# Performance work log

Hardware: AMD Instinct MI355X
Metric: run time of the kernel (lower is better)

## Reference

```python
import jax, jax.numpy as jnp
import numpy as np

B, S, D, H = 2, 2048, 1024, 16
DEPTH = D // H


def setup_inputs() -> dict:
    key = jax.random.key(0)
    ks = jax.random.split(key, 12)
    sc = 1.0 / np.sqrt(D)
    n = lambda k, shp, s=sc: jax.random.normal(k, shp, dtype=jnp.float32) * s
    return {
        "q": jax.random.normal(ks[0], (B, S, D), dtype=jnp.float32),
        "k": jax.random.normal(ks[1], (B, S, D), dtype=jnp.float32),
        "v": jax.random.normal(ks[2], (B, S, D), dtype=jnp.float32),
        # key-padding mask: 1 = masked, 0 = keep (added to logits * -1e9)
        "mask": (jax.random.uniform(ks[3], (B, 1, 1, S)) < 0.1).astype(jnp.float32),
        "wq_w": n(ks[4], (D, D)), "wq_b": jnp.zeros((D,), jnp.float32),
        "wk_w": n(ks[5], (D, D)), "wk_b": jnp.zeros((D,), jnp.float32),
        "wv_w": n(ks[6], (D, D)), "wv_b": jnp.zeros((D,), jnp.float32),
        "dense_w": n(ks[7], (D, D)), "dense_b": jnp.zeros((D,), jnp.float32),
    }


def _split_heads(x, b, s):
    # [B, S, D] -> [B, H, S, depth]
    return x.reshape(b, s, H, DEPTH).transpose(0, 2, 1, 3)


def reference(q, k, v, mask, wq_w, wq_b, wk_w, wk_b, wv_w, wv_b, dense_w, dense_b):
    b, sq, _ = q.shape
    sk = k.shape[1]
    qh = _split_heads(q @ wq_w.T + wq_b, b, sq)
    kh = _split_heads(k @ wk_w.T + wk_b, b, sk)
    vh = _split_heads(v @ wv_w.T + wv_b, b, sk)
    scale = 1.0 / jnp.sqrt(jnp.float32(DEPTH))
    logits = jnp.einsum('bhqd,bhkd->bhqk', qh, kh) * scale  # [B,H,Sq,Sk]
    logits = logits + mask * (-1e9)
    attn = jax.nn.softmax(logits, axis=-1)
    ctx = jnp.einsum('bhqk,bhkd->bhqd', attn, vh)
    ctx = ctx.transpose(0, 2, 1, 3).reshape(b, sq, D)  # concat heads
    out = ctx @ dense_w.T + dense_b
    return out, attn
```

## Files before the change

### kernel.cpp

```cpp
#include <hip/hip_runtime.h>

#define BB 2
#define SS 2048
#define DD 1024
#define HH 16
#define DEPTH 64
#define MTOT (BB*SS)
#define QW 8
#define QBLK (QW*16)
#define NT (SS/64)
#define NT2 (SS/128)
#define NPROJ ((size_t)BB*HH*SS*DEPTH)
#define WSZ   ((size_t)DD*DD)

using f16 = _Float16;
typedef _Float16 f16x8 __attribute__((ext_vector_type(8)));
typedef _Float16 f16x4 __attribute__((ext_vector_type(4)));
typedef float f32x4 __attribute__((ext_vector_type(4)));

#define LOG2E 1.44269504088896f
#define SC2   (0.125f * LOG2E)

#define GLOAD16(g, l) __builtin_amdgcn_global_load_lds(                      \
    (__attribute__((address_space(1))) const void*)(g),                      \
    (__attribute__((address_space(3))) void*)(l), 16, 0, 0)

#define BARV(N) do {                                                         \
    __builtin_amdgcn_sched_barrier(0);                                       \
    asm volatile("s_waitcnt vmcnt(" #N ") lgkmcnt(0)" ::: "memory");         \
    __builtin_amdgcn_sched_barrier(0);                                       \
    __builtin_amdgcn_s_barrier();                                            \
    __builtin_amdgcn_sched_barrier(0);                                       \
} while (0)

__global__ __launch_bounds__(256) void cvt_kernel(
    const float* __restrict__ q, const float* __restrict__ k, const float* __restrict__ v,
    const float* __restrict__ w0, const float* __restrict__ w1, const float* __restrict__ w2,
    f16* __restrict__ qf, f16* __restrict__ kf, f16* __restrict__ vf,
    f16* __restrict__ wq, f16* __restrict__ wk, f16* __restrict__ wv)
{
    const int z = blockIdx.y;
    const float* s = z==0?q : z==1?k : z==2?v : z==3?w0 : z==4?w1 : w2;
    f16*        d = z==0?qf: z==1?kf: z==2?vf: z==3?wq: z==4?wk: wv;
    const size_t n = (z < 3) ? NPROJ : WSZ;
    for (size_t i = ((size_t)blockIdx.x * 256 + threadIdx.x) * 8; i < n;
         i += (size_t)gridDim.x * 256 * 8) {
        f32x4 a = *(const f32x4*)(s + i);
        f32x4 b = *(const f32x4*)(s + i + 4);
        f16x8 o = {(f16)a[0], (f16)a[1], (f16)a[2], (f16)a[3],
                   (f16)b[0], (f16)b[1], (f16)b[2], (f16)b[3]};
        *(f16x8*)(d + i) = o;
    }
}

__global__ __launch_bounds__(256) void cvt2_kernel(
    const float* __restrict__ s, f16* __restrict__ d)
{
    size_t i = ((size_t)blockIdx.x * 256 + threadIdx.x) * 8;
    if (i < WSZ) {
        f32x4 a = *(const f32x4*)(s + i);
        f32x4 b = *(const f32x4*)(s + i + 4);
        f16x8 o = {(f16)a[0], (f16)a[1], (f16)a[2], (f16)a[3],
                   (f16)b[0], (f16)b[1], (f16)b[2], (f16)b[3]};
        *(f16x8*)(d + i) = o;
    }
}

__global__ __launch_bounds__(256, 4) void proj_kernel(
    const f16* __restrict__ qf, const f16* __restrict__ kf, const f16* __restrict__ vf,
    const f16* __restrict__ wqw, const f16* __restrict__ wkw, const f16* __restrict__ wvw,
    const float* __restrict__ bq, const float* __restrict__ bk, const float* __restrict__ bv,
    f16* __restrict__ qh, f16* __restrict__ kh, f16* __restrict__ vt)
{
    const int mode = blockIdx.z;
    const f16* A    = mode==0 ? qf  : mode==1 ? kf  : vf;
    const f16* Bw   = mode==0 ? wqw : mode==1 ? wkw : wvw;
    const float* bias = mode==0 ? bq : mode==1 ? bk : bv;

    __shared__ f16 As[128*64];
    __shared__ f16 Bs[128*64];

    const int tid = threadIdx.x, wave = tid >> 6, lane = tid & 63;
    const int m0 = blockIdx.y * 128, n0 = blockIdx.x * 128;
    const int wm = (wave >> 1) * 64, wn = (wave & 1) * 64;
    const int lrow = lane & 15, g = lane >> 4;
    const int sw = lrow & 7;
    const int srow = tid >> 3;
    const int schk = (tid & 7) ^ (srow & 7);

    f32x4 acc[4][4] = {};

    for (int kk = 0; kk < DD; kk += 64) {
        #pragma unroll
        for (int i = 0; i < 4; ++i) {
            GLOAD16(A  + (size_t)(m0 + i*32 + srow) * DD + kk + schk * 8,
                    &As[i*2048 + wave*512]);
            GLOAD16(Bw + (size_t)(n0 + i*32 + srow) * DD + kk + schk * 8,
                    &Bs[i*2048 + wave*512]);
        }
        __syncthreads();
        for (int kf2 = 0; kf2 < 2; ++kf2) {
            f16x8 a[4], bf[4];
            for (int i = 0; i < 4; ++i)
                a[i]  = *(const f16x8*)&As[(wm + i*16 + lrow)*64 + ((kf2*4 + g) ^ sw)*8];
            for (int i = 0; i < 4; ++i)
                bf[i] = *(const f16x8*)&Bs[(wn + i*16 + lrow)*64 + ((kf2*4 + g) ^ sw)*8];
            for (int mi = 0; mi < 4; ++mi)
                for (int ni = 0; ni < 4; ++ni)
                    acc[mi][ni] = __builtin_amdgcn_mfma_f32_16x16x32_f16(a[mi], bf[ni], acc[mi][ni], 0, 0, 0);
        }
        __syncthreads();
    }

    const int rbase = g * 4;
    if (mode == 2) {
        for (int ni = 0; ni < 4; ++ni) {
            int n = n0 + wn + ni * 16 + lrow;
            float bval = bias[n];
            int hh = n >> 6, dep = n & 63;
            for (int mi = 0; mi < 4; ++mi) {
                int m = m0 + wm + mi * 16 + rbase;
                int bb = m >> 11, s = m & 2047;
                f16x4 pk = {(f16)(acc[mi][ni][0] + bval), (f16)(acc[mi][ni][1] + bval),
                            (f16)(acc[mi][ni][2] + bval), (f16)(acc[mi][ni][3] + bval)};
                *(f16x4*)&vt[((size_t)(bb * HH + hh) * DEPTH + dep) * SS + s] = pk;
            }
        }
    } else {
        f16* dst = (mode == 0) ? qh : kh;
        for (int ni = 0; ni < 4; ++ni) {
            int n = n0 + wn + ni * 16 + lrow;
            float bval = bias[n];
            int hh = n >> 6, dep = n & 63;
            for (int mi = 0; mi < 4; ++mi)
                for (int j = 0; j < 4; ++j) {
                    int m = m0 + wm + mi * 16 + rbase + j;
                    int bb = m >> 11, s = m & 2047;
                    dst[((size_t)(bb * HH + hh) * SS + s) * DEPTH + dep] = (f16)(acc[mi][ni][j] + bval);
                }
        }
    }
}

__global__ __launch_bounds__(512, 4) void attn_kernel(
    const f16* __restrict__ qh, const f16* __restrict__ kh, const f16* __restrict__ vt,
    const float* __restrict__ mask, float* __restrict__ attn_out, f16* __restrict__ ctx)
{
    __shared__ unsigned char mflag[SS];
    __shared__ f16 Ks[3][64*64];
    __shared__ f16 Vs[3][64*64];
    __shared__ f16 Pl[QW][16][72];

    const int tid = threadIdx.x, wave = tid >> 6, lane = tid & 63;
    const int L = blockIdx.x;
    const int xcd = L & 7, iw = L >> 3;
    const int bh = xcd * 4 + (iw >> 4);
    const int qb = iw & 15;
    const int b = bh >> 4, h = bh & 15;
    const int q0 = qb * QBLK;
    const int lrow = lane & 15, g = lane >> 4;
    const int rbase = g * 4;
    const int sw = lrow & 7;
    const int srow = tid >> 3;
    const int schk = (tid & 7) ^ (srow & 7);

    const f16* Qbase = qh + (size_t)bh * SS * DEPTH;
    const f16* Kb = kh + (size_t)bh * SS * DEPTH;
    const f16* Vb = vt + (size_t)bh * DEPTH * SS;

    for (int i = tid; i < SS; i += 512)
        mflag[i] = mask[b * SS + i] > 0.5f ? 1 : 0;

    f16x8 aq[2];
    for (int kf2 = 0; kf2 < 2; ++kf2)
        aq[kf2] = *(const f16x8*)(Qbase + (size_t)(q0 + wave*16 + lrow) * DEPTH + kf2*32 + g*8);

    float s_l[4] = {0.f, 0.f, 0.f, 0.f};
    GLOAD16(Kb + (size_t)(srow) * DEPTH + schk * 8,        &Ks[0][wave * 512]);
    GLOAD16(Kb + (size_t)(64 + srow) * DEPTH + schk * 8,   &Vs[0][wave * 512]);
    GLOAD16(Kb + (size_t)(128 + srow) * DEPTH + schk * 8,  &Ks[1][wave * 512]);
    GLOAD16(Kb + (size_t)(192 + srow) * DEPTH + schk * 8,  &Vs[1][wave * 512]);
    __syncthreads();
    for (int t = 0; t < NT2; ++t) {
        const int cur = t % 3;
        const int nxt = (t + 2) % 3;
        const int t2 = (t + 2) & (NT2 - 1);
        GLOAD16(Kb + (size_t)(t2*128 + srow) * DEPTH + schk * 8,      &Ks[nxt][wave * 512]);
        GLOAD16(Kb + (size_t)(t2*128 + 64 + srow) * DEPTH + schk * 8, &Vs[nxt][wave * 512]);
        #pragma unroll
        for (int nf = 0; nf < 8; ++nf) {
            const f16* tb = (nf < 4) ? &Ks[cur][0] : &Vs[cur][0];
            const int nfl = nf & 3;
            f32x4 a4 = {};
            for (int kf2 = 0; kf2 < 2; ++kf2) {
                f16x8 bf = *(const f16x8*)&tb[(nfl*16 + lrow)*64 + ((kf2*4 + g) ^ sw)*8];
                a4 = __builtin_amdgcn_mfma_f32_16x16x32_f16(aq[kf2], bf, a4, 0, 0, 0);
            }
            float sel = mflag[t*128 + nf*16 + lrow] ? 0.f : 1.f;
            for (int j = 0; j < 4; ++j)
                s_l[j] += sel * __builtin_amdgcn_exp2f(a4[j] * SC2);
        }
        if (t < NT2 - 1) BARV(2);
        else __syncthreads();
    }
    for (int j = 0; j < 4; ++j) {
        float s = s_l[j];
        for (int off = 1; off < 16; off <<= 1) s += __shfl_xor(s, off);
        s_l[j] = 1.0f / s;
    }

    f32x4 cacc[4] = {};
    f32x4 st[4];
    float* arow = attn_out + ((size_t)bh * SS + q0 + wave * 16) * SS;
    GLOAD16(Kb + (size_t)(srow) * DEPTH + schk * 8,        &Ks[0][wave * 512]);
    GLOAD16(Vb + (size_t)srow * SS + 0 + schk * 8,         &Vs[0][wave * 512]);
    GLOAD16(Kb + (size_t)(64 + srow) * DEPTH + schk * 8,   &Ks[1][wave * 512]);
    GLOAD16(Vb + (size_t)srow * SS + 64 + schk * 8,        &Vs[1][wave * 512]);
    __syncthreads();
    for (int kt = 0; kt < NT; ++kt) {
        const int cur = kt % 3;
        const int nxt = (kt + 2) % 3;
        const int t2 = (kt + 2) & (NT - 1);
        if (kt > 0) {
            #pragma unroll
            for (int i = 0; i < 4; ++i) {
                int r = i * 4 + g;
                __builtin_nontemporal_store(st[i],
                    (f32x4*)&arow[(size_t)r * SS + (kt-1)*64 + lrow*4]);
            }
        }
        GLOAD16(Kb + (size_t)(t2*64 + srow) * DEPTH + schk * 8, &Ks[nxt][wave * 512]);
        GLOAD16(Vb + (size_t)srow * SS + t2*64 + schk * 8,      &Vs[nxt][wave * 512]);
        for (int nf = 0; nf < 4; ++nf) {
            f32x4 a4 = {};
            for (int kf2 = 0; kf2 < 2; ++kf2) {
                f16x8 bf = *(const f16x8*)&Ks[cur][(nf*16 + lrow)*64 + ((kf2*4 + g) ^ sw)*8];
                a4 = __builtin_amdgcn_mfma_f32_16x16x32_f16(aq[kf2], bf, a4, 0, 0, 0);
            }
            float sel = mflag[kt*64 + nf*16 + lrow] ? 0.f : 1.f;
            for (int j = 0; j < 4; ++j) {
                float p = sel * __builtin_amdgcn_exp2f(a4[j] * SC2) * s_l[j];
                Pl[wave][rbase + j][nf*16 + lrow] = (f16)p;
            }
        }
        for (int kf2 = 0; kf2 < 2; ++kf2) {
            f16x8 pa = *(const f16x8*)&Pl[wave][lrow][kf2*32 + g*8];
            for (int nf = 0; nf < 4; ++nf) {
                f16x8 bv = *(const f16x8*)&Vs[cur][(nf*16 + lrow)*64 + ((kf2*4 + g) ^ sw)*8];
                cacc[nf] = __builtin_amdgcn_mfma_f32_16x16x32_f16(pa, bv, cacc[nf], 0, 0, 0);
            }
        }
        #pragma unroll
        for (int i = 0; i < 4; ++i) {
            int r = i * 4 + g;
            f16x4 pv4 = *(const f16x4*)&Pl[wave][r][lrow * 4];
            st[i] = (f32x4){(float)pv4[0], (float)pv4[1], (float)pv4[2], (float)pv4[3]};
        }
        BARV(6);
    }
    #pragma unroll
    for (int i = 0; i < 4; ++i) {
        int r = i * 4 + g;
        __builtin_nontemporal_store(st[i],
            (f32x4*)&arow[(size_t)r * SS + (NT-1)*64 + lrow*4]);
    }
    for (int nf = 0; nf < 4; ++nf)
        for (int j = 0; j < 4; ++j) {
            int qrow = q0 + wave * 16 + rbase + j;
            ctx[((size_t)(b * SS + qrow) * HH + h) * DEPTH + nf*16 + lrow] = (f16)cacc[nf][j];
        }
}

__global__ __launch_bounds__(256, 4) void dense_kernel(
    const f16* __restrict__ ctx, const f16* __restrict__ W16,
    const float* __restrict__ bias, float* __restrict__ out)
{
    __shared__ f16 As[128*64];
    __shared__ f16 Bs[128*64];

    const int tid = threadIdx.x, wave = tid >> 6, lane = tid & 63;
    const int m0 = blockIdx.y * 128, n0 = blockIdx.x * 128;
    const int wm = (wave >> 1) * 64, wn = (wave & 1) * 64;
    const int lrow = lane & 15, g = lane >> 4;
    const int sw = lrow & 7;
    const int srow = tid >> 3;
    const int schk = (tid & 7) ^ (srow & 7);

    f32x4 acc[4][4] = {};

    for (int kk = 0; kk < DD; kk += 64) {
        #pragma unroll
        for (int i = 0; i < 4; ++i) {
            GLOAD16(ctx + (size_t)(m0 + i*32 + srow) * DD + kk + schk * 8,
                    &As[i*2048 + wave*512]);
            GLOAD16(W16 + (size_t)(n0 + i*32 + srow) * DD + kk + schk * 8,
                    &Bs[i*2048 + wave*512]);
        }
        __syncthreads();
        for (int kf2 = 0; kf2 < 2; ++kf2) {
            f16x8 a[4], bf[4];
            for (int i = 0; i < 4; ++i)
                a[i]  = *(const f16x8*)&As[(wm + i*16 + lrow)*64 + ((kf2*4 + g) ^ sw)*8];
            for (int i = 0; i < 4; ++i)
                bf[i] = *(const f16x8*)&Bs[(wn + i*16 + lrow)*64 + ((kf2*4 + g) ^ sw)*8];
            for (int mi = 0; mi < 4; ++mi)
                for (int ni = 0; ni < 4; ++ni)
                    acc[mi][ni] = __builtin_amdgcn_mfma_f32_16x16x32_f16(a[mi], bf[ni], acc[mi][ni], 0, 0, 0);
        }
        __syncthreads();
    }

    const int rbase = g * 4;
    for (int ni = 0; ni < 4; ++ni) {
        int n = n0 + wn + ni * 16 + lrow;
        float bval = bias[n];
        for (int mi = 0; mi < 4; ++mi)
            for (int j = 0; j < 4; ++j) {
                int m = m0 + wm + mi * 16 + rbase + j;
                out[(size_t)m * DD + n] = acc[mi][ni][j] + bval;
            }
    }
}

extern "C" void kernel_launch(void* const* d_in, const int* in_sizes, int n_in,
                              void* d_out, int out_size, void* d_ws, size_t ws_size,
                              hipStream_t stream) {
    const float* q       = (const float*)d_in[0];
    const float* k       = (const float*)d_in[1];
    const float* v       = (const float*)d_in[2];
    const float* mask    = (const float*)d_in[3];
    const float* wq_w    = (const float*)d_in[4];
    const float* wq_b    = (const float*)d_in[5];
    const float* wk_w    = (const float*)d_in[6];
    const float* wk_b    = (const float*)d_in[7];
    const float* wv_w    = (const float*)d_in[8];
    const float* wv_b    = (const float*)d_in[9];
    const float* dense_w = (const float*)d_in[10];
    const float* dense_b = (const float*)d_in[11];

    float* out  = (float*)d_out;
    float* attn = out + (size_t)MTOT * DD;

    f16* qh  = (f16*)d_ws;
    f16* kh  = qh + NPROJ;
    f16* vt  = kh + NPROJ;
    f16* ctx = vt + NPROJ;

    f16* sc   = (f16*)attn;
    f16* qf   = sc;
    f16* kf   = sc + NPROJ;
    f16* vf   = sc + 2*NPROJ;
    f16* wq16 = sc + 3*NPROJ;
    f16* wk16 = wq16 + WSZ;
    f16* wv16 = wk16 + WSZ;

    f16* dw16 = qh;

    cvt_kernel<<<dim3(1024, 6), 256, 0, stream>>>(q, k, v, wq_w, wk_w, wv_w,
                                                  qf, kf, vf, wq16, wk16, wv16);
    proj_kernel<<<dim3(8, 32, 3), 256, 0, stream>>>(qf, kf, vf, wq16, wk16, wv16,
                                                    wq_b, wk_b, wv_b, qh, kh, vt);
    attn_kernel<<<dim3(512), 512, 0, stream>>>(qh, kh, vt, mask, attn, ctx);
    cvt2_kernel<<<dim3(512), 256, 0, stream>>>(dense_w, dw16);
    dense_kernel<<<dim3(8, 32), 256, 0, stream>>>(ctx, dw16, dense_b, out);
}
```

Baseline: 218.9 us.

## Triple-buffer projection GEMM K-tiles with async global-to-LDS prefetch

Rewrites the projection GEMM main loop to use 32-wide K tiles in a three-deep LDS ring buffer. Loads for tile t+2 are issued while tile t is being computed, and vmcnt waits replace the full sync pair. The goal is to hide global load latency behind MFMA work, at the cost of a different swizzle and an occupancy hint lowered from 4 to 3 blocks. The loop issues wrapped-around prefetches on its last two iterations, which are then drained at the end of the kernel.

Result: no change. 220.7 us (+0.8%).

```diff
diff --git a/kernel.cpp b/kernel.cpp
--- a/kernel.cpp
+++ b/kernel.cpp
@@ -33,6 +33,8 @@
     __builtin_amdgcn_sched_barrier(0);                                       \
 } while (0)
 
+#define ENDDRAIN() asm volatile("s_waitcnt vmcnt(0)" ::: "memory")
+
 __global__ __launch_bounds__(256) void cvt_kernel(
     const float* __restrict__ q, const float* __restrict__ k, const float* __restrict__ v,
     const float* __restrict__ w0, const float* __restrict__ w1, const float* __restrict__ w2,
@@ -66,7 +68,7 @@
     }
 }
 
-__global__ __launch_bounds__(256, 4) void proj_kernel(
+__global__ __launch_bounds__(256, 3) void proj_kernel(
     const f16* __restrict__ qf, const f16* __restrict__ kf, const f16* __restrict__ vf,
     const f16* __restrict__ wqw, const f16* __restrict__ wkw, const f16* __restrict__ wvw,
     const float* __restrict__ bq, const float* __restrict__ bk, const float* __restrict__ bv,
@@ -77,40 +79,51 @@
     const f16* Bw   = mode==0 ? wqw : mode==1 ? wkw : wvw;
     const float* bias = mode==0 ? bq : mode==1 ? bk : bv;
 
-    __shared__ f16 As[128*64];
-    __shared__ f16 Bs[128*64];
+    __shared__ f16 As[3][128*32];
+    __shared__ f16 Bs[3][128*32];
 
     const int tid = threadIdx.x, wave = tid >> 6, lane = tid & 63;
     const int m0 = blockIdx.y * 128, n0 = blockIdx.x * 128;
     const int wm = (wave >> 1) * 64, wn = (wave & 1) * 64;
     const int lrow = lane & 15, g = lane >> 4;
-    const int sw = lrow & 7;
-    const int srow = tid >> 3;
-    const int schk = (tid & 7) ^ (srow & 7);
+    const int rchk = (lrow >> 1) & 3;
+    const int srow = tid >> 2;
+    const int schk = (tid & 3) ^ ((tid >> 3) & 3);
 
     f32x4 acc[4][4] = {};
 
-    for (int kk = 0; kk < DD; kk += 64) {
-        #pragma unroll
-        for (int i = 0; i < 4; ++i) {
-            GLOAD16(A  + (size_t)(m0 + i*32 + srow) * DD + kk + schk * 8,
-                    &As[i*2048 + wave*512]);
-            GLOAD16(Bw + (size_t)(n0 + i*32 + srow) * DD + kk + schk * 8,
-                    &Bs[i*2048 + wave*512]);
-        }
-        __syncthreads();
-        for (int kf2 = 0; kf2 < 2; ++kf2) {
-            f16x8 a[4], bf[4];
-            for (int i = 0; i < 4; ++i)
-                a[i]  = *(const f16x8*)&As[(wm + i*16 + lrow)*64 + ((kf2*4 + g) ^ sw)*8];
-            for (int i = 0; i < 4; ++i)
-                bf[i] = *(const f16x8*)&Bs[(wn + i*16 + lrow)*64 + ((kf2*4 + g) ^ sw)*8];
-            for (int mi = 0; mi < 4; ++mi)
-                for (int ni = 0; ni < 4; ++ni)
-                    acc[mi][ni] = __builtin_amdgcn_mfma_f32_16x16x32_f16(a[mi], bf[ni], acc[mi][ni], 0, 0, 0);
-        }
-        __syncthreads();
-    }
+    auto stage = [&](int t, int buf) {
+        const int kk = t * 32;
+        #pragma unroll
+        for (int s2 = 0; s2 < 2; ++s2) {
+            GLOAD16(A  + (size_t)(m0 + s2*64 + srow) * DD + kk + schk * 8,
+                    &As[buf][s2*2048 + wave*512]);
+            GLOAD16(Bw + (size_t)(n0 + s2*64 + srow) * DD + kk + schk * 8,
+                    &Bs[buf][s2*2048 + wave*512]);
+        }
+    };
+
+    stage(0, 0);
+    stage(1, 1);
+    BARV(4);
+    for (int t = 0; t < DD/32; ++t) {
+        const int cur = t % 3;
+        const int nxt = (t + 2) % 3;
+        const int t2 = (t + 2) & (DD/32 - 1);
+        stage(t2, nxt);
+        f16x8 a[4], bf[4];
+        #pragma unroll
+        for (int i = 0; i < 4; ++i)
+            a[i]  = *(const f16x8*)&As[cur][(wm + i*16 + lrow)*32 + (g ^ rchk)*8];
+        #pragma unroll
+        for (int i = 0; i < 4; ++i)
+            bf[i] = *(const f16x8*)&Bs[cur][(wn + i*16 + lrow)*32 + (g ^ rchk)*8];
+        for (int mi = 0; mi < 4; ++mi)
+            for (int ni = 0; ni < 4; ++ni)
+                acc[mi][ni] = __builtin_amdgcn_mfma_f32_16x16x32_f16(a[mi], bf[ni], acc[mi][ni], 0, 0, 0);
+        BARV(4);
+    }
+    ENDDRAIN();
 
     const int rbase = g * 4;
     if (mode == 2) {
@@ -269,6 +282,7 @@
             int qrow = q0 + wave * 16 + rbase + j;
             ctx[((size_t)(b * SS + qrow) * HH + h) * DEPTH + nf*16 + lrow] = (f16)cacc[nf][j];
         }
+    ENDDRAIN();
 }
 
 __global__ __launch_bounds__(256, 4) void dense_kernel(
```
